# Performance work log

Hardware: AMD Instinct MI355X
Metric: run time of the kernel (lower is better)

## Reference

```python
import jax, jax.numpy as jnp
import numpy as np

B, S, D, H = 8, 2048, 1024, 16
HD = D // H          # head_dim = 64
HID = 4 * HD         # hidden = 256
MAX_LR = 0.01
NUM_LAYERS = 2


def _split_heads(x):
    b, s, _ = x.shape
    return x.reshape(b, s, H, HD).transpose(0, 2, 1, 3).reshape(b * H, s, HD)


def _merge_heads(x, b):
    return x.reshape(b, H, -1, HD).transpose(0, 2, 1, 3).reshape(b, -1, D)


def _rmsnorm_w(x, w, eps=1e-6):
    # learned RMSNorm: x / rms(x) * w
    return x * w * jax.lax.rsqrt(jnp.mean(x * x, axis=-1, keepdims=True) + eps)


def _pf_rmsnorm(h):
    # parameter-free RMSNorm, returns (h_norm, rms)
    rms = jnp.sqrt(jnp.mean(h * h, axis=-1, keepdims=True) + 1e-8)
    return h / rms, rms


def _pf_rmsnorm_bwd(d_out, h_norm, rms):
    d = d_out.shape[-1]
    dy = jnp.sum(d_out * h_norm, axis=-1, keepdims=True)
    return (d_out - h_norm * dy / d) / rms


def _gelu_grad(x):
    cdf = 0.5 * (1.0 + jax.lax.erf(x * 0.7071067811865476))
    pdf = jnp.exp(-0.5 * x * x) * 0.3989422804014327
    return cdf + x * pdf


def _memory_forward(x, Ws):
    h = x
    n = len(Ws)
    for i, W in enumerate(Ws):
        h = jnp.matmul(h, W)  # (BH,S,din) @ (BH,din,dout)
        if i < n - 1:
            h = jax.nn.gelu(h, approximate=False)
    h = jnp.nan_to_num(h, nan=0.0, posinf=0.0, neginf=0.0)
    h_norm, _ = _pf_rmsnorm(h)
    return h_norm + x


def _memory_grad(keys, values, theta, Ws):
    Ws = [jax.lax.stop_gradient(W) for W in Ws]  # detach fast weights
    acts = [keys]
    pres = []
    h = keys
    n = len(Ws)
    for i, W in enumerate(Ws):
        pre = jnp.matmul(h, W)
        pres.append(pre)
        h = jax.nn.gelu(pre, approximate=False) if i < n - 1 else pre
        acts.append(h)
    h_norm, rms = _pf_rmsnorm(acts[-1])
    pred = h_norm + keys
    d_pred = 2.0 * theta[..., None] * (pred - values)
    d_h = _pf_rmsnorm_bwd(d_pred, h_norm, rms)
    grads = [None] * n
    for i in range(n - 1, -1, -1):
        grads[i] = jnp.einsum('bsi,bso->bio', acts[i], d_h)
        if i > 0:
            d_h = jnp.matmul(d_h, Ws[i].transpose(0, 2, 1)) * _gelu_grad(pres[i - 1])
    return grads


def _clip_grads(grads, max_norm=10.0):
    sq = sum(jnp.sum(g.reshape(g.shape[0], -1) ** 2, axis=1) for g in grads)
    coef = jnp.minimum(max_norm / (jnp.sqrt(sq) + 1e-6), 1.0)
    coef = jax.lax.stop_gradient(coef)[:, None, None]
    return [g * coef for g in grads]


def reference(x, W_K, W_V, W_Q, mem_W0, mem_W1, k_norm_w, q_norm_w,
              store_norm_w, retrieve_norm_w, alpha_w, alpha_b,
              theta_w, theta_b, eta_w, eta_b):
    b = x.shape[0]
    bh = b * H
    # init per-sample fast weights and zero momentum
    Ws = [jnp.broadcast_to(mem_W0, (bh,) + mem_W0.shape),
          jnp.broadcast_to(mem_W1, (bh,) + mem_W1.shape)]
    mom = [jnp.zeros_like(W) for W in Ws]
    # ---- update(x, ms, mom) ----
    x_n = _rmsnorm_w(x, store_norm_w)
    keys = _rmsnorm_w(_split_heads(x_n @ W_K), k_norm_w)
    values = _split_heads(x_n @ W_V)
    alpha = jax.nn.sigmoid(x_n @ alpha_w + alpha_b)          # (B,S,H)
    theta = jax.nn.sigmoid(x_n @ theta_w + theta_b) * MAX_LR
    eta = jax.nn.sigmoid(x_n @ eta_w + eta_b)
    to_bh = lambda t: t.transpose(0, 2, 1).reshape(bh, -1)   # (BH,S)
    alpha, theta, eta = to_bh(alpha), to_bh(theta), to_bh(eta)
    grads = _clip_grads(_memory_grad(keys, values, theta, Ws))
    a_mean = jnp.mean(alpha, axis=1)[:, None, None]
    e_mean = jnp.mean(eta, axis=1)[:, None, None]
    new_Ws = []
    for W, m, g in zip(Ws, mom, grads):
        new_m = e_mean * m - g
        new_w = (1.0 - a_mean) * W + new_m
        new_w = jnp.where(jnp.isfinite(new_w), new_w, jax.lax.stop_gradient(W))
        new_Ws.append(new_w)
    # ---- retrieve(x, new_ms) ----
    q = _rmsnorm_w(_split_heads(_rmsnorm_w(x, retrieve_norm_w) @ W_Q), q_norm_w)
    out = _memory_forward(q, new_Ws)
    return _merge_heads(out, b)


def setup_inputs() -> dict:
    key = jax.random.key(0)
    ks = jax.random.split(key, 12)
    xav0 = float(np.sqrt(2.0 / (HD + HID)))
    xav1 = float(np.sqrt(2.0 / (HID + HD)))
    return {
        'x': jax.random.normal(ks[0], (B, S, D), jnp.float32),
        'W_K': jax.random.normal(ks[1], (D, D), jnp.float32) / np.float32(np.sqrt(D)),
        'W_V': jax.random.normal(ks[2], (D, D), jnp.float32) / np.float32(np.sqrt(D)),
        'W_Q': jax.random.normal(ks[3], (D, D), jnp.float32) / np.float32(np.sqrt(D)),
        'mem_W0': jax.random.normal(ks[4], (HD, HID), jnp.float32) * xav0,
        'mem_W1': jax.random.normal(ks[5], (HID, HD), jnp.float32) * xav1,
        'k_norm_w': jnp.ones((HD,), jnp.float32),
        'q_norm_w': jnp.ones((HD,), jnp.float32),
        'store_norm_w': jnp.ones((D,), jnp.float32),
        'retrieve_norm_w': jnp.ones((D,), jnp.float32),
        'alpha_w': jax.random.normal(ks[6], (D, H), jnp.float32) * 0.01,
        'alpha_b': jnp.full((H,), -5.0, jnp.float32),
        'theta_w': jax.random.normal(ks[7], (D, H), jnp.float32) * 0.01,
        'theta_b': jnp.full((H,), -3.0, jnp.float32),
        'eta_w': jax.random.normal(ks[8], (D, H), jnp.float32) * 0.01,
        'eta_b': jnp.zeros((H,), jnp.float32),
    }
```

## Files before the change

kernel.cpp:

```cpp
#include <hip/hip_runtime.h>

typedef unsigned short u16;
typedef unsigned int   u32;

#define DEV static __device__ __forceinline__

constexpr int S    = 2048;
constexpr int D    = 1024;
constexpr int H    = 16;
constexpr int BB   = 8;
constexpr int BH   = BB * H;
constexpr int BS   = BB * S;
constexpr long NR  = (long)BH * S;

typedef __attribute__((ext_vector_type(8))) short bf16x8;
typedef __attribute__((ext_vector_type(4))) float f32x4;

DEV float b2f(u16 u) { return __uint_as_float(((u32)u) << 16); }
DEV u16   f2b(float f) {
  u32 x = __float_as_uint(f);
  u32 r = (x + 0x7fffu + ((x >> 16) & 1u)) >> 16;
  return (u16)r;
}
DEV float geluf(float x) { return 0.5f * x * (1.0f + erff(x * 0.70710678118654752440f)); }
DEV float sigmoidf(float z) { return 1.0f / (1.0f + expf(-z)); }
DEV float wsum(float v) {
#pragma unroll
  for (int o = 32; o > 0; o >>= 1) v += __shfl_xor(v, o, 64);
  return v;
}
DEV float rsum16(float v) {
  v += __shfl_xor(v, 1, 64);
  v += __shfl_xor(v, 2, 64);
  v += __shfl_xor(v, 4, 64);
  v += __shfl_xor(v, 8, 64);
  return v;
}
DEV float nan0(float v) {
  u32 b = __float_as_uint(v);
  return ((b & 0x7f800000u) == 0x7f800000u) ? 0.f : v;
}
DEV bool finitef(float v) {
  u32 b = __float_as_uint(v);
  return (b & 0x7f800000u) != 0x7f800000u;
}
DEV void dma16(const void* g, void* l) {
  __builtin_amdgcn_global_load_lds((const __attribute__((address_space(1))) void*)g,
                                   (__attribute__((address_space(3))) void*)l, 16, 0, 0);
}
DEV int swz4(int r) { return (r ^ (r >> 2)) & 3; }

template <bool FIRST>
__global__ void k_xnorm(const float* __restrict__ x, const float* __restrict__ cw,
                        float* __restrict__ rinv, u16* __restrict__ xb) {
  int row  = blockIdx.x * 4 + (threadIdx.x >> 6);
  int lane = threadIdx.x & 63;
  const float* p = x + (size_t)row * D;
  float4 v[4];
#pragma unroll
  for (int j = 0; j < 4; j++) v[j] = *(const float4*)(p + lane * 4 + j * 256);
  float rs;
  if (FIRST) {
    float s = 0.f;
#pragma unroll
    for (int j = 0; j < 4; j++)
      s += v[j].x * v[j].x + v[j].y * v[j].y + v[j].z * v[j].z + v[j].w * v[j].w;
    s = wsum(s);
    rs = rsqrtf(s * (1.0f / D) + 1e-6f);
    if (lane == 0) rinv[row] = rs;
  } else {
    rs = rinv[row];
  }
#pragma unroll
  for (int j = 0; j < 4; j++) {
    float4 w4 = *(const float4*)(cw + lane * 4 + j * 256);
    ushort4 o;
    o.x = f2b(v[j].x * rs * w4.x);
    o.y = f2b(v[j].y * rs * w4.y);
    o.z = f2b(v[j].z * rs * w4.z);
    o.w = f2b(v[j].w * rs * w4.w);
    *(ushort4*)&xb[(size_t)row * D + lane * 4 + j * 256] = o;
  }
}

__global__ void k_wtrans(const float* __restrict__ W0, const float* __restrict__ W1,
                         const float* __restrict__ W2, u16* __restrict__ WT) {
  __shared__ float tl[64][65];
  const float* W = blockIdx.z == 0 ? W0 : blockIdx.z == 1 ? W1 : W2;
  u16* dst = WT + (size_t)blockIdx.z * D * D;
  int bx = blockIdx.x, by = blockIdx.y;
  int t = threadIdx.x;
  int r = t >> 6, c = t & 63;
#pragma unroll
  for (int i = 0; i < 64; i += 4)
    tl[i + r][c] = W[(size_t)(bx * 64 + i + r) * D + by * 64 + c];
  __syncthreads();
#pragma unroll
  for (int i = 0; i < 64; i += 4)
    dst[(size_t)(by * 64 + i + r) * D + bx * 64 + c] = f2b(tl[c][i + r]);
}

__global__ void k_atw(const float* __restrict__ aw, const float* __restrict__ tw,
                      u16* __restrict__ atw) {
  int idx = blockIdx.x * 256 + threadIdx.x;
  int n = idx >> 10, k = idx & 1023;
  float v = (n < 16) ? aw[(size_t)k * 16 + n] : tw[(size_t)k * 16 + (n - 16)];
  atw[idx] = f2b(v);
}

template <bool NORM>
__global__ __launch_bounds__(256) void k_proj_mfma(
    const u16* __restrict__ xb, const u16* __restrict__ WT,
    const float* __restrict__ hw, u16* __restrict__ outp) {
  __shared__ u16 As[128 * 32];
  __shared__ u16 Bs[128 * 32];
  int t = threadIdx.x;
  int wave = t >> 6, lane = t & 63;
  int wm = wave >> 1, wn = wave & 1;
  int m0 = blockIdx.y * 128, n0 = blockIdx.x * 128;
  int quad = lane >> 4, l15 = lane & 15;
  int rl = lane >> 2;
  int q  = (lane & 3) ^ swz4(rl);

  f32x4 acc[4][4] = {};

  int aoff[4], boff[4];
#pragma unroll
  for (int f = 0; f < 4; f++) {
    aoff[f] = (wm * 64 + f * 16 + l15) * 32 + (quad ^ swz4(l15)) * 8;
    boff[f] = (wn * 64 + f * 16 + l15) * 32 + (quad ^ swz4(l15)) * 8;
  }
  const u16* ga0 = xb + (size_t)(m0 + wave * 32 + rl) * D + q * 8;
  const u16* ga1 = ga0 + 16 * D;
  const u16* gb0 = WT + (size_t)(n0 + wave * 32 + rl) * D + q * 8;
  const u16* gb1 = gb0 + 16 * D;
  u16* lA0 = &As[(wave * 32) * 32];
  u16* lA1 = &As[(wave * 32 + 16) * 32];
  u16* lB0 = &Bs[(wave * 32) * 32];
  u16* lB1 = &Bs[(wave * 32 + 16) * 32];

  for (int k0 = 0; k0 < D; k0 += 32) {
    dma16(ga0 + k0, lA0);
    dma16(ga1 + k0, lA1);
    dma16(gb0 + k0, lB0);
    dma16(gb1 + k0, lB1);
    __syncthreads();
    bf16x8 af[4], bfr[4];
#pragma unroll
    for (int f = 0; f < 4; f++) {
      af[f]  = *(const bf16x8*)&As[aoff[f]];
      bfr[f] = *(const bf16x8*)&Bs[boff[f]];
    }
#pragma unroll
    for (int i = 0; i < 4; i++)
#pragma unroll
      for (int j = 0; j < 4; j++)
        acc[i][j] = __builtin_amdgcn_mfma_f32_16x16x32_bf16(af[i], bfr[j], acc[i][j], 0, 0, 0);
    __syncthreads();
  }

  int h = blockIdx.x * 2 + wn;
  float hwv[4];
  if (NORM) {
#pragma unroll
    for (int f = 0; f < 4; f++) hwv[f] = hw[f * 16 + l15];
  }
#pragma unroll
  for (int fm = 0; fm < 4; fm++) {
    f32x4 rn = {};
    if (NORM) {
      f32x4 ss = acc[fm][0] * acc[fm][0] + acc[fm][1] * acc[fm][1] +
                 acc[fm][2] * acc[fm][2] + acc[fm][3] * acc[fm][3];
#pragma unroll
      for (int c = 0; c < 4; c++) {
        float s = rsum16(ss[c]);
        rn[c] = rsqrtf(s * (1.f / 64) + 1e-6f);
      }
    }
#pragma unroll
    for (int r = 0; r < 4; r++) {
      int gr = m0 + wm * 64 + fm * 16 + quad * 4 + r;
      int b = gr >> 11, s_ = gr & 2047;
      size_t base = ((size_t)(b * 16 + h) * S + s_) * 64 + l15;
#pragma unroll
      for (int fn = 0; fn < 4; fn++) {
        float v = acc[fm][fn][r];
        if (NORM) v *= rn[r] * hwv[fn];
        outp[base + fn * 16] = f2b(v);
      }
    }
  }
}

__global__ __launch_bounds__(256) void k_ate2(
    const u16* __restrict__ xb, const u16* __restrict__ atw,
    const float* __restrict__ ab, const float* __restrict__ tb,
    float* __restrict__ alpha, float* __restrict__ theta) {
  __shared__ u16 As[2][128 * 32];
  __shared__ u16 Bs[2][32 * 32];
  int t = threadIdx.x;
  int wave = t >> 6, lane = t & 63;
  int m0 = blockIdx.x * 128;
  int quad = lane >> 4, l15 = lane & 15;
  int rl = lane >> 2;
  int q = (lane & 3) ^ swz4(rl);

  f32x4 acc[2][2] = {};
  int aoff[2], boff[2];
#pragma unroll
  for (int f = 0; f < 2; f++) {
    aoff[f] = (wave * 32 + f * 16 + l15) * 32 + (quad ^ swz4(l15)) * 8;
    boff[f] = (f * 16 + l15) * 32 + (quad ^ swz4(l15)) * 8;
  }
  const u16* ga0 = xb + (size_t)(m0 + wave * 32 + rl) * D + q * 8;
  const u16* ga1 = ga0 + 16 * D;
  const u16* gb = atw + (size_t)((wave & 1) * 16 + rl) * D + (wave >> 1) * 32 + q * 8;
  u16* lA0h0 = &As[0][(wave * 32) * 32];
  u16* lA1h0 = &As[0][(wave * 32 + 16) * 32];
  u16* lA0h1 = &As[1][(wave * 32) * 32];
  u16* lA1h1 = &As[1][(wave * 32 + 16) * 32];
  u16* lB    = &Bs[wave >> 1][((wave & 1) * 16) * 32];

  for (int k0 = 0; k0 < D; k0 += 64) {
    dma16(ga0 + k0, lA0h0);
    dma16(ga1 + k0, lA1h0);
    dma16(ga0 + k0 + 32, lA0h1);
    dma16(ga1 + k0 + 32, lA1h1);
    dma16(gb + k0, lB);
    __syncthreads();
#pragma unroll
    for (int h = 0; h < 2; h++) {
      bf16x8 af[2], bfr[2];
#pragma unroll
      for (int f = 0; f < 2; f++) {
        af[f]  = *(const bf16x8*)&As[h][aoff[f]];
        bfr[f] = *(const bf16x8*)&Bs[h][boff[f]];
      }
#pragma unroll
      for (int i = 0; i < 2; i++)
#pragma unroll
        for (int j = 0; j < 2; j++)
          acc[i][j] = __builtin_amdgcn_mfma_f32_16x16x32_bf16(af[i], bfr[j], acc[i][j], 0, 0, 0);
    }
    __syncthreads();
  }

#pragma unroll
  for (int fn = 0; fn < 2; fn++) {
    float bias = (fn == 0) ? ab[l15] : tb[l15];
    float scale = (fn == 0) ? 1.f : 0.01f;
    float* dst = (fn == 0) ? alpha : theta;
#pragma unroll
    for (int fm = 0; fm < 2; fm++) {
#pragma unroll
      for (int r = 0; r < 4; r++) {
        int gr = m0 + wave * 32 + fm * 16 + quad * 4 + r;
        int b = gr >> 11, s_ = gr & 2047;
        float v = sigmoidf(acc[fm][fn][r] + bias) * scale;
        dst[(long)(b * 16 + l15) * S + s_] = v;
      }
    }
  }
}

__global__ void k_mean(const float* __restrict__ alpha, float* __restrict__ amean) {
  int bh = blockIdx.x, t = threadIdx.x;
  float sa = 0.f;
  for (int i = t; i < S; i += 256) sa += alpha[(long)bh * S + i];
  sa = wsum(sa);
  __shared__ float sh[4];
  int w = t >> 6, lane = t & 63;
  if (lane == 0) sh[w] = sa;
  __syncthreads();
  if (t == 0) amean[bh] = (sh[0] + sh[1] + sh[2] + sh[3]) * (1.f / S);
}

__global__ void k_wsmall(const float* __restrict__ W0, const float* __restrict__ W1,
                         u16* __restrict__ W0T, u16* __restrict__ W1b, u16* __restrict__ W1T) {
  int idx = blockIdx.x * 256 + threadIdx.x;
  int sec = blockIdx.y;
  if (sec == 0) {
    int k = idx & 63, i = idx >> 6;
    W0T[idx] = f2b(W0[k * 256 + i]);
  } else if (sec == 1) {
    W1b[idx] = f2b(W1[idx]);
  } else {
    int i = idx & 255, o = idx >> 8;
    W1T[idx] = f2b(W1[i * 64 + o]);
  }
}

__global__ void k_keysT(const u16* __restrict__ keysg, u16* __restrict__ blk) {
  long idx = (long)blockIdx.x * 256 + threadIdx.x;
  int col = (int)(idx & 63);
  long s = (idx >> 6) * 4;
  ushort4 o;
  o.x = keysg[(size_t)s * 64 + col];
  o.y = keysg[(size_t)(s + 1) * 64 + col];
  o.z = keysg[(size_t)(s + 2) * 64 + col];
  o.w = keysg[(size_t)(s + 3) * 64 + col];
  *(ushort4*)&blk[((size_t)(s >> 4) * 4 + (col >> 4)) * 256 + (col & 15) * 16 + (s & 15)] = o;
}

__global__ __launch_bounds__(512, 2) void kfuse(
    const u16* __restrict__ keysv, const u16* __restrict__ vals,
    const u16* __restrict__ keysTb,
    const u16* __restrict__ W0T, const u16* __restrict__ W1T,
    const u16* __restrict__ W1b, const float* __restrict__ theta,
    float* __restrict__ g0t, float* __restrict__ g1t) {
  __shared__ u16 L[57344];
  u16* S1   = L;
  u16* W0sL = L + 32768;
  u16* dhR  = L + 32768;
  u16* dhblk = L + 40960;
  u16* Kblk = L + 49152;

  int t = threadIdx.x;
  int w = t >> 6, lane = t & 63;
  int quad = lane >> 4, l15 = lane & 15;
  int bh = blockIdx.y, strip = blockIdx.x;
  long grow = (long)bh * S + strip * 128;
  int bswz = (quad ^ swz4(l15)) * 8;

  {
    const u16* ksrc = keysTb + (grow >> 4) * 1024 + (size_t)w * 1024 + lane * 8;
    dma16(ksrc, Kblk + w * 1024);
    dma16(ksrc + 512, Kblk + w * 1024 + 512);
    int i = t >> 1, c = t & 1;
    int key = swz4(i & 15);
    const u16* gsrc = W0T + i * 64 + c * 32;
    u16* ldst = W0sL + c * 8192 + i * 32;
#pragma unroll
    for (int j = 0; j < 4; j++)
      *(bf16x8*)&ldst[j * 8] = *(const bf16x8*)&gsrc[(j ^ key) * 8];
  }
  __syncthreads();

  f32x4 acc2[4];
  ushort4 gpr[16];
  {
    f32x4 acc[16] = {};
    bf16x8 afA[2];
#pragma unroll
    for (int kc = 0; kc < 2; kc++) {
      union { bf16x8 v; u16 e[8]; } u;
#pragma unroll
      for (int j = 0; j < 8; j++) {
        int k = kc * 32 + quad * 8 + j;
        u.e[j] = Kblk[(w * 4 + (k >> 4)) * 256 + (k & 15) * 16 + l15];
      }
      afA[kc] = u.v;
    }
#pragma unroll
    for (int f = 0; f < 16; f++) {
      bf16x8 b0 = *(const bf16x8*)&W0sL[(f * 16 + l15) * 32 + bswz];
      bf16x8 b1 = *(const bf16x8*)&W0sL[8192 + (f * 16 + l15) * 32 + bswz];
      acc[f] = __builtin_amdgcn_mfma_f32_16x16x32_bf16(afA[0], b0, acc[f], 0, 0, 0);
      acc[f] = __builtin_amdgcn_mfma_f32_16x16x32_bf16(afA[1], b1, acc[f], 0, 0, 0);
    }
    __syncthreads();

#pragma unroll
    for (int f = 0; f < 16; f++) {
      ushort4 oa, og;
#pragma unroll
      for (int r = 0; r < 4; r++) {
        float v = acc[f][r];
        float cdf = 0.5f * (1.0f + erff(v * 0.70710678118654752440f));
        float pdf = expf(-0.5f * v * v) * 0.3989422804014327f;
        ((u16*)&oa)[r] = f2b(v * cdf);
        ((u16*)&og)[r] = f2b(cdf + v * pdf);
      }
      *(ushort4*)&S1[(w * 16 + f) * 256 + l15 * 16 + quad * 4] = oa;
      gpr[f] = og;
    }
  }

  {
#pragma unroll
    for (int fn = 0; fn < 4; fn++) acc2[fn] = (f32x4){};
#pragma unroll
    for (int kc = 0; kc < 8; kc++) {
      union { bf16x8 v; u16 e[8]; } u;
#pragma unroll
      for (int j = 0; j < 8; j++) {
        int c = kc * 32 + quad * 8 + j;
        u.e[j] = S1[(w * 16 + (c >> 4)) * 256 + (c & 15) * 16 + l15];
      }
#pragma unroll
      for (int fn = 0; fn < 4; fn++) {
        bf16x8 bv = *(const bf16x8*)&W1T[(size_t)(fn * 16 + l15) * 256 + kc * 32 + quad * 8];
        acc2[fn] = __builtin_amdgcn_mfma_f32_16x16x32_bf16(u.v, bv, acc2[fn], 0, 0, 0);
      }
    }
  }

  {
    f32x4 ss = acc2[0] * acc2[0] + acc2[1] * acc2[1] +
               acc2[2] * acc2[2] + acc2[3] * acc2[3];
    f32x4 rrms, th2;
    long rowg0 = grow + w * 16 + quad * 4;
#pragma unroll
    for (int r = 0; r < 4; r++) {
      float s = rsum16(ss[r]);
      rrms[r] = rsqrtf(s * (1.f / 64) + 1e-8f);
      th2[r] = 2.f * theta[rowg0 + r];
    }
    f32x4 hn[4], dp[4];
    f32x4 dyp = {};
#pragma unroll
    for (int fn = 0; fn < 4; fn++) {
      int col = fn * 16 + l15;
#pragma unroll
      for (int r = 0; r < 4; r++) {
        float h = acc2[fn][r] * rrms[r];
        float k = b2f(keysv[(rowg0 + r) * 64 + col]);
        float v = b2f(vals[(rowg0 + r) * 64 + col]);
        float d = th2[r] * (h + k - v);
        hn[fn][r] = h;
        dp[fn][r] = d;
        dyp[r] += d * h;
      }
    }
#pragma unroll
    for (int r = 0; r < 4; r++) dyp[r] = rsum16(dyp[r]);
#pragma unroll
    for (int fn = 0; fn < 4; fn++) {
      int col = fn * 16 + l15;
      ushort4 ob;
#pragma unroll
      for (int r = 0; r < 4; r++) {
        float d = (dp[fn][r] - hn[fn][r] * dyp[r] * (1.f / 64)) * rrms[r];
        u16 db = f2b(d);
        ((u16*)&ob)[r] = db;
        int row = w * 16 + quad * 4 + r;
        int g = ((col >> 3) & 3) ^ swz4(row & 15);
        dhR[(col >> 5) * 4096 + row * 32 + g * 8 + (col & 7)] = db;
      }
      *(ushort4*)&dhblk[(w * 4 + fn) * 256 + l15 * 16 + quad * 4] = ob;
    }
  }
  __syncthreads();

  {
    int qh = quad >> 1, ql = (quad & 1) * 8;
    f32x4 a3[4][2] = {};
#pragma unroll
    for (int ks = 0; ks < 4; ks++) {
      int s16 = ks * 2 + qh;
      bf16x8 af[4], bf2[2];
#pragma unroll
      for (int m = 0; m < 4; m++)
        af[m] = *(const bf16x8*)&dhblk[(s16 * 4 + m) * 256 + l15 * 16 + ql];
#pragma unroll
      for (int f2 = 0; f2 < 2; f2++)
        bf2[f2] = *(const bf16x8*)&S1[(s16 * 16 + w * 2 + f2) * 256 + l15 * 16 + ql];
#pragma unroll
      for (int m = 0; m < 4; m++)
#pragma unroll
        for (int f2 = 0; f2 < 2; f2++)
          a3[m][f2] = __builtin_amdgcn_mfma_f32_16x16x32_bf16(af[m], bf2[f2], a3[m][f2], 0, 0, 0);
    }
    float* gp1 = g1t + (size_t)bh * 16384;
#pragma unroll
    for (int m = 0; m < 4; m++)
#pragma unroll
      for (int f2 = 0; f2 < 2; f2++) {
        int n = w * 32 + f2 * 16 + l15;
#pragma unroll
        for (int r = 0; r < 4; r++)
          atomicAdd(&gp1[(size_t)(m * 16 + quad * 4 + r) * 256 + n], a3[m][f2][r]);
      }
  }
  __syncthreads();

  {
    f32x4 a5[16] = {};
    bf16x8 afd[2];
#pragma unroll
    for (int kc = 0; kc < 2; kc++)
      afd[kc] = *(const bf16x8*)&dhR[kc * 4096 + (w * 16 + l15) * 32 + bswz];
#pragma unroll
    for (int f = 0; f < 16; f++) {
#pragma unroll
      for (int kc = 0; kc < 2; kc++) {
        bf16x8 bv = *(const bf16x8*)&W1b[(size_t)(f * 16 + l15) * 64 + kc * 32 + quad * 8];
        a5[f] = __builtin_amdgcn_mfma_f32_16x16x32_bf16(afd[kc], bv, a5[f], 0, 0, 0);
      }
    }
#pragma unroll
    for (int f = 0; f < 16; f++) {
      ushort4 od;
#pragma unroll
      for (int r = 0; r < 4; r++)
        ((u16*)&od)[r] = f2b(a5[f][r] * b2f(((u16*)&gpr[f])[r]));
      *(ushort4*)&S1[(w * 16 + f) * 256 + l15 * 16 + quad * 4] = od;
    }
  }
  __syncthreads();

  {
    int qh = quad >> 1, ql = (quad & 1) * 8;
    f32x4 a6[4][2] = {};
#pragma unroll
    for (int ks = 0; ks < 4; ks++) {
      int s16 = ks * 2 + qh;
      bf16x8 af[4], bf2[2];
#pragma unroll
      for (int m = 0; m < 4; m++)
        af[m] = *(const bf16x8*)&Kblk[(s16 * 4 + m) * 256 + l15 * 16 + ql];
#pragma unroll
      for (int f2 = 0; f2 < 2; f2++)
        bf2[f2] = *(const bf16x8*)&S1[(s16 * 16 + w * 2 + f2) * 256 + l15 * 16 + ql];
#pragma unroll
      for (int m = 0; m < 4; m++)
#pragma unroll
        for (int f2 = 0; f2 < 2; f2++)
          a6[m][f2] = __builtin_amdgcn_mfma_f32_16x16x32_bf16(af[m], bf2[f2], a6[m][f2], 0, 0, 0);
    }
    float* gp0 = g0t + (size_t)bh * 16384;
#pragma unroll
    for (int m = 0; m < 4; m++)
#pragma unroll
      for (int f2 = 0; f2 < 2; f2++) {
        int n = w * 32 + f2 * 16 + l15;
#pragma unroll
        for (int r = 0; r < 4; r++)
          atomicAdd(&gp0[(size_t)(m * 16 + quad * 4 + r) * 256 + n], a6[m][f2][r]);
      }
  }
}

__global__ __launch_bounds__(512, 2) void kret(
    const u16* __restrict__ qp, const u16* __restrict__ qTb,
    const u16* __restrict__ nW0T, const u16* __restrict__ nW1T,
    float* __restrict__ outp) {
  __shared__ u16 L[57344];
  u16* S1   = L;
  u16* W0sL = L + 32768;
  u16* Kblk = L + 49152;

  int t = threadIdx.x;
  int w = t >> 6, lane = t & 63;
  int quad = lane >> 4, l15 = lane & 15;
  int bh = blockIdx.y, strip = blockIdx.x;
  long grow = (long)bh * S + strip * 128;
  int bswz = (quad ^ swz4(l15)) * 8;

  {
    const u16* ksrc = qTb + (grow >> 4) * 1024 + (size_t)w * 1024 + lane * 8;
    dma16(ksrc, Kblk + w * 1024);
    dma16(ksrc + 512, Kblk + w * 1024 + 512);
    int i = t >> 1, c = t & 1;
    int key = swz4(i & 15);
    const u16* gsrc = nW0T + (size_t)bh * 16384 + i * 64 + c * 32;
    u16* ldst = W0sL + c * 8192 + i * 32;
#pragma unroll
    for (int j = 0; j < 4; j++)
      *(bf16x8*)&ldst[j * 8] = *(const bf16x8*)&gsrc[(j ^ key) * 8];
  }
  __syncthreads();

  {
    f32x4 acc[16] = {};
    bf16x8 afA[2];
#pragma unroll
    for (int kc = 0; kc < 2; kc++) {
      union { bf16x8 v; u16 e[8]; } u;
#pragma unroll
      for (int j = 0; j < 8; j++) {
        int k = kc * 32 + quad * 8 + j;
        u.e[j] = Kblk[(w * 4 + (k >> 4)) * 256 + (k & 15) * 16 + l15];
      }
      afA[kc] = u.v;
    }
#pragma unroll
    for (int f = 0; f < 16; f++) {
      bf16x8 b0 = *(const bf16x8*)&W0sL[(f * 16 + l15) * 32 + bswz];
      bf16x8 b1 = *(const bf16x8*)&W0sL[8192 + (f * 16 + l15) * 32 + bswz];
      acc[f] = __builtin_amdgcn_mfma_f32_16x16x32_bf16(afA[0], b0, acc[f], 0, 0, 0);
      acc[f] = __builtin_amdgcn_mfma_f32_16x16x32_bf16(afA[1], b1, acc[f], 0, 0, 0);
    }
#pragma unroll
    for (int f = 0; f < 16; f++) {
      ushort4 oa;
#pragma unroll
      for (int r = 0; r < 4; r++) ((u16*)&oa)[r] = f2b(geluf(acc[f][r]));
      *(ushort4*)&S1[(w * 16 + f) * 256 + l15 * 16 + quad * 4] = oa;
    }
  }

  f32x4 acc2[4];
#pragma unroll
  for (int fn = 0; fn < 4; fn++) acc2[fn] = (f32x4){};
  const u16* W1p = nW1T + (size_t)bh * 16384;
#pragma unroll
  for (int kc = 0; kc < 8; kc++) {
    union { bf16x8 v; u16 e[8]; } u;
#pragma unroll
    for (int j = 0; j < 8; j++) {
      int c = kc * 32 + quad * 8 + j;
      u.e[j] = S1[(w * 16 + (c >> 4)) * 256 + (c & 15) * 16 + l15];
    }
#pragma unroll
    for (int fn = 0; fn < 4; fn++) {
      bf16x8 bv = *(const bf16x8*)&W1p[(size_t)(fn * 16 + l15) * 256 + kc * 32 + quad * 8];
      acc2[fn] = __builtin_amdgcn_mfma_f32_16x16x32_bf16(u.v, bv, acc2[fn], 0, 0, 0);
    }
  }

  {
    f32x4 hv[4];
    f32x4 ss = {};
#pragma unroll
    for (int fn = 0; fn < 4; fn++) {
#pragma unroll
      for (int r = 0; r < 4; r++) {
        float v = nan0(acc2[fn][r]);
        hv[fn][r] = v;
        ss[r] += v * v;
      }
    }
    f32x4 rrms;
#pragma unroll
    for (int r = 0; r < 4; r++) {
      float s = rsum16(ss[r]);
      rrms[r] = rsqrtf(s * (1.f / 64) + 1e-8f);
    }
    long b = bh >> 4, hh = bh & 15;
#pragma unroll
    for (int r = 0; r < 4; r++) {
      long s_ = strip * 128 + w * 16 + quad * 4 + r;
      long gr = grow + w * 16 + quad * 4 + r;
      size_t obase = (size_t)(b * S + s_) * D + hh * 64;
#pragma unroll
      for (int fn = 0; fn < 4; fn++) {
        int col = fn * 16 + l15;
        outp[obase + col] = hv[fn][r] * rrms[r] + b2f(qp[gr * 64 + col]);
      }
    }
  }
}

__global__ void k_zero(float* __restrict__ p, long n) {
  long i = (long)blockIdx.x * 256 + threadIdx.x;
  if (i < n) p[i] = 0.f;
}

__global__ void k_clip(const float* __restrict__ g0, const float* __restrict__ g1,
                       float* __restrict__ coef) {
  int bh = blockIdx.x, t = threadIdx.x;
  const float* p0 = g0 + (long)bh * 16384;
  const float* p1 = g1 + (long)bh * 16384;
  float s = 0.f;
  for (int i = t; i < 16384; i += 256) {
    float a = p0[i]; s += a * a;
    float b = p1[i]; s += b * b;
  }
  s = wsum(s);
  __shared__ float sh[4];
  int w = t >> 6, lane = t & 63;
  if (lane == 0) sh[w] = s;
  __syncthreads();
  if (t == 0) {
    float tot = sh[0] + sh[1] + sh[2] + sh[3];
    float c = 10.f / (sqrtf(tot) + 1e-6f);
    coef[bh] = fminf(c, 1.f);
  }
}

__global__ void k_updT(const float* __restrict__ W0, const float* __restrict__ W1,
                       const float* __restrict__ g0t, const float* __restrict__ g1t,
                       const float* __restrict__ amean, const float* __restrict__ coef,
                       u16* __restrict__ nW0T, u16* __restrict__ nW1T) {
  long i = (long)blockIdx.x * 256 + threadIdx.x;
  int half = (int)(i >> 21);
  long j = i & ((1L << 21) - 1);
  int bh = (int)(j >> 14);
  int idx = (int)(j & 16383);
  float a = 1.f - amean[bh], cf = coef[bh];
  if (half == 0) {
    int k = idx & 63, ii = idx >> 6;
    float w = W0[k * 256 + ii];
    float nw = a * w - cf * g0t[(long)bh * 16384 + k * 256 + ii];
    if (!finitef(nw)) nw = w;
    nW0T[j] = f2b(nw);
  } else {
    int ii = idx & 255, o = idx >> 8;
    float w = W1[ii * 64 + o];
    float nw = a * w - cf * g1t[(long)bh * 16384 + idx];
    if (!finitef(nw)) nw = w;
    nW1T[j] = f2b(nw);
  }
}

extern "C" void kernel_launch(void* const* d_in, const int* in_sizes, int n_in,
                              void* d_out, int out_size, void* d_ws, size_t ws_size,
                              hipStream_t stream) {
  const float* x   = (const float*)d_in[0];
  const float* W_K = (const float*)d_in[1];
  const float* W_V = (const float*)d_in[2];
  const float* W_Q = (const float*)d_in[3];
  const float* mW0 = (const float*)d_in[4];
  const float* mW1 = (const float*)d_in[5];
  const float* knw = (const float*)d_in[6];
  const float* qnw = (const float*)d_in[7];
  const float* snw = (const float*)d_in[8];
  const float* rnw = (const float*)d_in[9];
  const float* aw  = (const float*)d_in[10];
  const float* ab  = (const float*)d_in[11];
  const float* tw  = (const float*)d_in[12];
  const float* tb  = (const float*)d_in[13];
  float* out = (float*)d_out;
  (void)ws_size; (void)in_sizes; (void)n_in; (void)out_size;

  char* w = (char*)d_ws;
  auto alloc = [&](size_t bytes) {
    char* p = w;
    w += (bytes + 255) / 256 * 256;
    return p;
  };
  float* rinv   = (float*)alloc((size_t)BS * 4);
  u16*   xs     = (u16*)alloc((size_t)BS * D * 2);
  u16*   WTb    = (u16*)alloc((size_t)3 * D * D * 2);
  u16*   keys   = (u16*)alloc(NR * 64 * 2);
  u16*   vals   = (u16*)alloc(NR * 64 * 2);
  float* alpha  = (float*)alloc(NR * 4);
  float* theta  = (float*)alloc(NR * 4);
  float* amean  = (float*)alloc(BH * 4);
  float* coef   = (float*)alloc(BH * 4);
  u16*   W0T    = (u16*)alloc(16384 * 2);
  u16*   W1b    = (u16*)alloc(16384 * 2);
  u16*   W1T    = (u16*)alloc(16384 * 2);
  u16*   atw    = (u16*)alloc((size_t)32 * D * 2);
  u16*   keysTb = (u16*)alloc(NR * 64 * 2);
  float* g0t    = (float*)alloc((size_t)BH * 16384 * 4);
  float* g1t    = (float*)alloc((size_t)BH * 16384 * 4);
  u16*   nW0T   = (u16*)alloc((size_t)BH * 16384 * 2);
  u16*   nW1T   = (u16*)alloc((size_t)BH * 16384 * 2);

  k_xnorm<true><<<BS / 4, 256, 0, stream>>>(x, snw, rinv, xs);
  k_wtrans<<<dim3(16, 16, 3), 256, 0, stream>>>(W_K, W_V, W_Q, WTb);
  k_atw<<<128, 256, 0, stream>>>(aw, tw, atw);
  k_proj_mfma<true><<<dim3(8, 128), 256, 0, stream>>>(xs, WTb, knw, keys);
  k_proj_mfma<false><<<dim3(8, 128), 256, 0, stream>>>(xs, WTb + (size_t)D * D, nullptr, vals);
  k_ate2<<<BS / 128, 256, 0, stream>>>(xs, atw, ab, tb, alpha, theta);
  k_mean<<<BH, 256, 0, stream>>>(alpha, amean);
  k_wsmall<<<dim3(64, 3), 256, 0, stream>>>(mW0, mW1, W0T, W1b, W1T);
  k_zero<<<(int)((2L * BH * 16384 + 255) / 256), 256, 0, stream>>>(g0t, 2L * BH * 16384);

  k_keysT<<<(int)(NR / 16), 256, 0, stream>>>(keys, keysTb);
  kfuse<<<dim3(16, BH), 512, 0, stream>>>(keys, vals, keysTb, W0T, W1T, W1b,
                                          theta, g0t, g1t);

  k_clip<<<BH, 256, 0, stream>>>(g0t, g1t, coef);
  k_updT<<<(int)(2L * BH * 16384 / 256), 256, 0, stream>>>(
      mW0, mW1, g0t, g1t, amean, coef, nW0T, nW1T);

  k_xnorm<false><<<BS / 4, 256, 0, stream>>>(x, rnw, rinv, xs);
  u16* q = keys;
  k_proj_mfma<true><<<dim3(8, 128), 256, 0, stream>>>(xs, WTb + (size_t)2 * D * D, qnw, q);
  k_keysT<<<(int)(NR / 16), 256, 0, stream>>>(q, keysTb);
  kret<<<dim3(16, BH), 512, 0, stream>>>(q, keysTb, nW0T, nW1T, out);
}
```

Before: 899.7 us.

## Load MFMA operands directly from global memory, shrink LDS, drop query transpose

In kfuse and kret the first-layer A operands (keys/queries) and W0 B operands are now read directly from global memory in row-major form instead of being staged into shared memory. This removes a staging barrier and the swizzled LDS copies. kfuse now reads the transposed-keys operand for the W0 gradient from global memory, and kret no longer needs the k_keysT transpose launch for queries. LDS use drops to 80KB and 64KB per block, which may let more blocks fit per CU. The cost is uncached global loads in the MFMA loops and a strided gather from dhblk in place of the dedicated dhR layout.

```diff
diff --git a/kernel.cpp b/kernel.cpp
--- a/kernel.cpp
+++ b/kernel.cpp
@@ -308,58 +308,30 @@
     const u16* __restrict__ W0T, const u16* __restrict__ W1T,
     const u16* __restrict__ W1b, const float* __restrict__ theta,
     float* __restrict__ g0t, float* __restrict__ g1t) {
-  __shared__ u16 L[57344];
-  u16* S1   = L;
-  u16* W0sL = L + 32768;
-  u16* dhR  = L + 32768;
-  u16* dhblk = L + 40960;
-  u16* Kblk = L + 49152;
+  __shared__ u16 L[40960];
+  u16* S1    = L;
+  u16* dhblk = L + 32768;
 
   int t = threadIdx.x;
   int w = t >> 6, lane = t & 63;
   int quad = lane >> 4, l15 = lane & 15;
   int bh = blockIdx.y, strip = blockIdx.x;
   long grow = (long)bh * S + strip * 128;
-  int bswz = (quad ^ swz4(l15)) * 8;
-
-  {
-    const u16* ksrc = keysTb + (grow >> 4) * 1024 + (size_t)w * 1024 + lane * 8;
-    dma16(ksrc, Kblk + w * 1024);
-    dma16(ksrc + 512, Kblk + w * 1024 + 512);
-    int i = t >> 1, c = t & 1;
-    int key = swz4(i & 15);
-    const u16* gsrc = W0T + i * 64 + c * 32;
-    u16* ldst = W0sL + c * 8192 + i * 32;
-#pragma unroll
-    for (int j = 0; j < 4; j++)
-      *(bf16x8*)&ldst[j * 8] = *(const bf16x8*)&gsrc[(j ^ key) * 8];
-  }
-  __syncthreads();
 
   f32x4 acc2[4];
   ushort4 gpr[16];
   {
     f32x4 acc[16] = {};
-    bf16x8 afA[2];
-#pragma unroll
-    for (int kc = 0; kc < 2; kc++) {
-      union { bf16x8 v; u16 e[8]; } u;
-#pragma unroll
-      for (int j = 0; j < 8; j++) {
-        int k = kc * 32 + quad * 8 + j;
-        u.e[j] = Kblk[(w * 4 + (k >> 4)) * 256 + (k & 15) * 16 + l15];
-      }
-      afA[kc] = u.v;
-    }
+    const u16* krow = keysv + (grow + w * 16 + l15) * 64 + quad * 8;
+    bf16x8 afA0 = *(const bf16x8*)(krow);
+    bf16x8 afA1 = *(const bf16x8*)(krow + 32);
 #pragma unroll
     for (int f = 0; f < 16; f++) {
-      bf16x8 b0 = *(const bf16x8*)&W0sL[(f * 16 + l15) * 32 + bswz];
-      bf16x8 b1 = *(const bf16x8*)&W0sL[8192 + (f * 16 + l15) * 32 + bswz];
-      acc[f] = __builtin_amdgcn_mfma_f32_16x16x32_bf16(afA[0], b0, acc[f], 0, 0, 0);
-      acc[f] = __builtin_amdgcn_mfma_f32_16x16x32_bf16(afA[1], b1, acc[f], 0, 0, 0);
-    }
-    __syncthreads();
-
+      bf16x8 b0 = *(const bf16x8*)&W0T[(f * 16 + l15) * 64 + quad * 8];
+      bf16x8 b1 = *(const bf16x8*)&W0T[(f * 16 + l15) * 64 + 32 + quad * 8];
+      acc[f] = __builtin_amdgcn_mfma_f32_16x16x32_bf16(afA0, b0, acc[f], 0, 0, 0);
+      acc[f] = __builtin_amdgcn_mfma_f32_16x16x32_bf16(afA1, b1, acc[f], 0, 0, 0);
+    }
 #pragma unroll
     for (int f = 0; f < 16; f++) {
       ushort4 oa, og;
@@ -426,16 +398,11 @@
     for (int r = 0; r < 4; r++) dyp[r] = rsum16(dyp[r]);
 #pragma unroll
     for (int fn = 0; fn < 4; fn++) {
-      int col = fn * 16 + l15;
       ushort4 ob;
 #pragma unroll
       for (int r = 0; r < 4; r++) {
         float d = (dp[fn][r] - hn[fn][r] * dyp[r] * (1.f / 64)) * rrms[r];
-        u16 db = f2b(d);
-        ((u16*)&ob)[r] = db;
-        int row = w * 16 + quad * 4 + r;
-        int g = ((col >> 3) & 3) ^ swz4(row & 15);
-        dhR[(col >> 5) * 4096 + row * 32 + g * 8 + (col & 7)] = db;
+        ((u16*)&ob)[r] = f2b(d);
       }
       *(ushort4*)&dhblk[(w * 4 + fn) * 256 + l15 * 16 + quad * 4] = ob;
     }
@@ -478,8 +445,15 @@
     f32x4 a5[16] = {};
     bf16x8 afd[2];
 #pragma unroll
-    for (int kc = 0; kc < 2; kc++)
-      afd[kc] = *(const bf16x8*)&dhR[kc * 4096 + (w * 16 + l15) * 32 + bswz];
+    for (int kc = 0; kc < 2; kc++) {
+      union { bf16x8 v; u16 e[8]; } u;
+#pragma unroll
+      for (int j = 0; j < 8; j++) {
+        int col = kc * 32 + quad * 8 + j;
+        u.e[j] = dhblk[(w * 4 + (col >> 4)) * 256 + (col & 15) * 16 + l15];
+      }
+      afd[kc] = u.v;
+    }
 #pragma unroll
     for (int f = 0; f < 16; f++) {
 #pragma unroll
@@ -501,6 +475,7 @@
 
   {
     int qh = quad >> 1, ql = (quad & 1) * 8;
+    const u16* Kg = keysTb + (size_t)(grow >> 4) * 1024;
     f32x4 a6[4][2] = {};
 #pragma unroll
     for (int ks = 0; ks < 4; ks++) {
@@ -508,7 +483,7 @@
       bf16x8 af[4], bf2[2];
 #pragma unroll
       for (int m = 0; m < 4; m++)
-        af[m] = *(const bf16x8*)&Kblk[(s16 * 4 + m) * 256 + l15 * 16 + ql];
+        af[m] = *(const bf16x8*)&Kg[(size_t)(s16 * 4 + m) * 256 + l15 * 16 + ql];
 #pragma unroll
       for (int f2 = 0; f2 < 2; f2++)
         bf2[f2] = *(const bf16x8*)&S1[(s16 * 16 + w * 2 + f2) * 256 + l15 * 16 + ql];
@@ -532,54 +507,28 @@
 }
 
 __global__ __launch_bounds__(512, 2) void kret(
-    const u16* __restrict__ qp, const u16* __restrict__ qTb,
-    const u16* __restrict__ nW0T, const u16* __restrict__ nW1T,
-    float* __restrict__ outp) {
-  __shared__ u16 L[57344];
-  u16* S1   = L;
-  u16* W0sL = L + 32768;
-  u16* Kblk = L + 49152;
+    const u16* __restrict__ qp, const u16* __restrict__ nW0T,
+    const u16* __restrict__ nW1T, float* __restrict__ outp) {
+  __shared__ u16 S1[32768];
 
   int t = threadIdx.x;
   int w = t >> 6, lane = t & 63;
   int quad = lane >> 4, l15 = lane & 15;
   int bh = blockIdx.y, strip = blockIdx.x;
   long grow = (long)bh * S + strip * 128;
-  int bswz = (quad ^ swz4(l15)) * 8;
-
-  {
-    const u16* ksrc = qTb + (grow >> 4) * 1024 + (size_t)w * 1024 + lane * 8;
-    dma16(ksrc, Kblk + w * 1024);
-    dma16(ksrc + 512, Kblk + w * 1024 + 512);
-    int i = t >> 1, c = t & 1;
-    int key = swz4(i & 15);
-    const u16* gsrc = nW0T + (size_t)bh * 16384 + i * 64 + c * 32;
-    u16* ldst = W0sL + c * 8192 + i * 32;
-#pragma unroll
-    for (int j = 0; j < 4; j++)
-      *(bf16x8*)&ldst[j * 8] = *(const bf16x8*)&gsrc[(j ^ key) * 8];
-  }
-  __syncthreads();
 
   {
     f32x4 acc[16] = {};
-    bf16x8 afA[2];
-#pragma unroll
-    for (int kc = 0; kc < 2; kc++) {
-      union { bf16x8 v; u16 e[8]; } u;
-#pragma unroll
-      for (int j = 0; j < 8; j++) {
-        int k = kc * 32 + quad * 8 + j;
-        u.e[j] = Kblk[(w * 4 + (k >> 4)) * 256 + (k & 15) * 16 + l15];
-      }
-      afA[kc] = u.v;
-    }
+    const u16* qrow = qp + (grow + w * 16 + l15) * 64 + quad * 8;
+    bf16x8 afA0 = *(const bf16x8*)(qrow);
+    bf16x8 afA1 = *(const bf16x8*)(qrow + 32);
+    const u16* W0p = nW0T + (size_t)bh * 16384;
 #pragma unroll
     for (int f = 0; f < 16; f++) {
-      bf16x8 b0 = *(const bf16x8*)&W0sL[(f * 16 + l15) * 32 + bswz];
-      bf16x8 b1 = *(const bf16x8*)&W0sL[8192 + (f * 16 + l15) * 32 + bswz];
-      acc[f] = __builtin_amdgcn_mfma_f32_16x16x32_bf16(afA[0], b0, acc[f], 0, 0, 0);
-      acc[f] = __builtin_amdgcn_mfma_f32_16x16x32_bf16(afA[1], b1, acc[f], 0, 0, 0);
+      bf16x8 b0 = *(const bf16x8*)&W0p[(f * 16 + l15) * 64 + quad * 8];
+      bf16x8 b1 = *(const bf16x8*)&W0p[(f * 16 + l15) * 64 + 32 + quad * 8];
+      acc[f] = __builtin_amdgcn_mfma_f32_16x16x32_bf16(afA0, b0, acc[f], 0, 0, 0);
+      acc[f] = __builtin_amdgcn_mfma_f32_16x16x32_bf16(afA1, b1, acc[f], 0, 0, 0);
     }
 #pragma unroll
     for (int f = 0; f < 16; f++) {
@@ -760,6 +709,5 @@
   k_xnorm<false><<<BS / 4, 256, 0, stream>>>(x, rnw, rinv, xs);
   u16* q = keys;
   k_proj_mfma<true><<<dim3(8, 128), 256, 0, stream>>>(xs, WTb + (size_t)2 * D * D, qnw, q);
-  k_keysT<<<(int)(NR / 16), 256, 0, stream>>>(q, keysTb);
-  kret<<<dim3(16, BH), 512, 0, stream>>>(q, keysTb, nW0T, nW1T, out);
-}
+  kret<<<dim3(16, BH), 512, 0, stream>>>(q, nW0T, nW1T, out);
+}
```

Result: slower. 923.8 us (+2.7%).

## Swizzle projection GEMM block order and drop query transpose in retrieval

Applied to the files above, without the earlier changes.

The projection GEMM now uses a 1D grid with a remapping from block id to tile, so consecutive blocks share the same weight column tile and improve L2 reuse. The retrieval kernel now loads query MFMA operands and the updated W0 fragments straight from global memory instead of staging them through a transposed copy and LDS. This removes the k_keysT launch before retrieval and shrinks kret's shared memory. The cost is uncoalesced global loads for the fragments in place of LDS reads.

```diff
diff --git a/kernel.cpp b/kernel.cpp
--- a/kernel.cpp
+++ b/kernel.cpp
@@ -117,7 +117,10 @@
   int t = threadIdx.x;
   int wave = t >> 6, lane = t & 63;
   int wm = wave >> 1, wn = wave & 1;
-  int m0 = blockIdx.y * 128, n0 = blockIdx.x * 128;
+  int bid = blockIdx.x;
+  int swz = (bid & 7) * 128 + (bid >> 3);
+  int mb = swz >> 3, nb = swz & 7;
+  int m0 = mb * 128, n0 = nb * 128;
   int quad = lane >> 4, l15 = lane & 15;
   int rl = lane >> 2;
   int q  = (lane & 3) ^ swz4(rl);
@@ -159,7 +162,7 @@
     __syncthreads();
   }
 
-  int h = blockIdx.x * 2 + wn;
+  int h = nb * 2 + wn;
   float hwv[4];
   if (NORM) {
 #pragma unroll
@@ -532,54 +535,28 @@
 }
 
 __global__ __launch_bounds__(512, 2) void kret(
-    const u16* __restrict__ qp, const u16* __restrict__ qTb,
-    const u16* __restrict__ nW0T, const u16* __restrict__ nW1T,
-    float* __restrict__ outp) {
-  __shared__ u16 L[57344];
-  u16* S1   = L;
-  u16* W0sL = L + 32768;
-  u16* Kblk = L + 49152;
+    const u16* __restrict__ qp, const u16* __restrict__ nW0T,
+    const u16* __restrict__ nW1T, float* __restrict__ outp) {
+  __shared__ u16 S1[32768];
 
   int t = threadIdx.x;
   int w = t >> 6, lane = t & 63;
   int quad = lane >> 4, l15 = lane & 15;
   int bh = blockIdx.y, strip = blockIdx.x;
   long grow = (long)bh * S + strip * 128;
-  int bswz = (quad ^ swz4(l15)) * 8;
-
-  {
-    const u16* ksrc = qTb + (grow >> 4) * 1024 + (size_t)w * 1024 + lane * 8;
-    dma16(ksrc, Kblk + w * 1024);
-    dma16(ksrc + 512, Kblk + w * 1024 + 512);
-    int i = t >> 1, c = t & 1;
-    int key = swz4(i & 15);
-    const u16* gsrc = nW0T + (size_t)bh * 16384 + i * 64 + c * 32;
-    u16* ldst = W0sL + c * 8192 + i * 32;
-#pragma unroll
-    for (int j = 0; j < 4; j++)
-      *(bf16x8*)&ldst[j * 8] = *(const bf16x8*)&gsrc[(j ^ key) * 8];
-  }
-  __syncthreads();
 
   {
     f32x4 acc[16] = {};
-    bf16x8 afA[2];
-#pragma unroll
-    for (int kc = 0; kc < 2; kc++) {
-      union { bf16x8 v; u16 e[8]; } u;
-#pragma unroll
-      for (int j = 0; j < 8; j++) {
-        int k = kc * 32 + quad * 8 + j;
-        u.e[j] = Kblk[(w * 4 + (k >> 4)) * 256 + (k & 15) * 16 + l15];
-      }
-      afA[kc] = u.v;
-    }
+    const u16* qrow = qp + (grow + w * 16 + l15) * 64 + quad * 8;
+    bf16x8 afA0 = *(const bf16x8*)(qrow);
+    bf16x8 afA1 = *(const bf16x8*)(qrow + 32);
+    const u16* W0p = nW0T + (size_t)bh * 16384;
 #pragma unroll
     for (int f = 0; f < 16; f++) {
-      bf16x8 b0 = *(const bf16x8*)&W0sL[(f * 16 + l15) * 32 + bswz];
-      bf16x8 b1 = *(const bf16x8*)&W0sL[8192 + (f * 16 + l15) * 32 + bswz];
-      acc[f] = __builtin_amdgcn_mfma_f32_16x16x32_bf16(afA[0], b0, acc[f], 0, 0, 0);
-      acc[f] = __builtin_amdgcn_mfma_f32_16x16x32_bf16(afA[1], b1, acc[f], 0, 0, 0);
+      bf16x8 b0 = *(const bf16x8*)&W0p[(f * 16 + l15) * 64 + quad * 8];
+      bf16x8 b1 = *(const bf16x8*)&W0p[(f * 16 + l15) * 64 + 32 + quad * 8];
+      acc[f] = __builtin_amdgcn_mfma_f32_16x16x32_bf16(afA0, b0, acc[f], 0, 0, 0);
+      acc[f] = __builtin_amdgcn_mfma_f32_16x16x32_bf16(afA1, b1, acc[f], 0, 0, 0);
     }
 #pragma unroll
     for (int f = 0; f < 16; f++) {
@@ -742,8 +719,8 @@
   k_xnorm<true><<<BS / 4, 256, 0, stream>>>(x, snw, rinv, xs);
   k_wtrans<<<dim3(16, 16, 3), 256, 0, stream>>>(W_K, W_V, W_Q, WTb);
   k_atw<<<128, 256, 0, stream>>>(aw, tw, atw);
-  k_proj_mfma<true><<<dim3(8, 128), 256, 0, stream>>>(xs, WTb, knw, keys);
-  k_proj_mfma<false><<<dim3(8, 128), 256, 0, stream>>>(xs, WTb + (size_t)D * D, nullptr, vals);
+  k_proj_mfma<true><<<1024, 256, 0, stream>>>(xs, WTb, knw, keys);
+  k_proj_mfma<false><<<1024, 256, 0, stream>>>(xs, WTb + (size_t)D * D, nullptr, vals);
   k_ate2<<<BS / 128, 256, 0, stream>>>(xs, atw, ab, tb, alpha, theta);
   k_mean<<<BH, 256, 0, stream>>>(alpha, amean);
   k_wsmall<<<dim3(64, 3), 256, 0, stream>>>(mW0, mW1, W0T, W1b, W1T);
@@ -759,7 +736,6 @@
 
   k_xnorm<false><<<BS / 4, 256, 0, stream>>>(x, rnw, rinv, xs);
   u16* q = keys;
-  k_proj_mfma<true><<<dim3(8, 128), 256, 0, stream>>>(xs, WTb + (size_t)2 * D * D, qnw, q);
-  k_keysT<<<(int)(NR / 16), 256, 0, stream>>>(q, keysTb);
-  kret<<<dim3(16, BH), 512, 0, stream>>>(q, keysTb, nW0T, nW1T, out);
-}
+  k_proj_mfma<true><<<1024, 256, 0, stream>>>(xs, WTb + (size_t)2 * D * D, qnw, q);
+  kret<<<dim3(16, BH), 512, 0, stream>>>(q, nW0T, nW1T, out);
+}
```

Measured after the change: 855.5 us. 4.9% less time.
